# Kernel tuning notes

Measured on AMD Instinct MI355X. Metric: run time of the kernel, lower is better.

## Reference

```python
import jax, jax.numpy as jnp
import numpy as np

IN_FEATURES = 4096
OUT_FEATURES = 4096
TOKENS = 8192
QMAX = 127.0


def setup_inputs() -> dict:
    key = jax.random.key(0)
    k1, k2, k3, k4 = jax.random.split(key, 4)
    x = jax.random.normal(k1, (TOKENS, IN_FEATURES), dtype=jnp.float32)
    # int8 quantized weights in [-127, 127]
    Wq = jax.random.randint(k2, (OUT_FEATURES, IN_FEATURES), -127, 128, dtype=jnp.int32).astype(jnp.int8)
    # per-row absmax scales (positive)
    row_scales = jax.random.uniform(k3, (OUT_FEATURES,), dtype=jnp.float32, minval=0.01, maxval=1.0)
    bias_param = jax.random.normal(k4, (OUT_FEATURES,), dtype=jnp.float32)
    return {"x": x, "Wq": Wq, "row_scales": row_scales, "bias_param": bias_param}


def reference(x, Wq, row_scales, bias_param):
    # rowwise dequant: W[o, i] = Wq[o, i] * row_scales[o] / 127
    W_dequant = Wq.astype(x.dtype) * (row_scales.astype(x.dtype) / QMAX)[:, None]  # [O, I]
    Y = jnp.matmul(x, W_dequant.T)  # [T, O]
    return Y + bias_param.astype(x.dtype)
```

## Files before the change

### kernel.cpp

```cpp
#include <hip/hip_runtime.h>

#define M_TOK 8192
#define N_OUT 4096
#define K_IN  4096

#define AS1 __attribute__((address_space(1)))
#define AS3 __attribute__((address_space(3)))

typedef __attribute__((ext_vector_type(4))) int i32x4;
typedef __attribute__((ext_vector_type(16))) int i32x16;

template <int OFF>
__device__ __forceinline__ i32x4 dsri(unsigned addr) {
    i32x4 r;
    asm volatile("ds_read_b128 %0, %1 offset:%2" : "=v"(r) : "v"(addr), "n"(OFF));
    return r;
}


__global__ __launch_bounds__(256) void quant_x_kernel(
    const float* __restrict__ x, signed char* __restrict__ xq,
    float* __restrict__ tok_scale)
{
    const int row = blockIdx.x;
    const float4* xr = reinterpret_cast<const float4*>(x + (size_t)row * K_IN);
    const int t = threadIdx.x;
    float4 v[4];
    float m = 0.f;
#pragma unroll
    for (int i = 0; i < 4; ++i) {
        v[i] = xr[t + 256 * i];
        m = fmaxf(m, fmaxf(fmaxf(fabsf(v[i].x), fabsf(v[i].y)),
                           fmaxf(fabsf(v[i].z), fabsf(v[i].w))));
    }
#pragma unroll
    for (int off = 32; off >= 1; off >>= 1)
        m = fmaxf(m, __shfl_xor(m, off, 64));
    __shared__ float wmax[4];
    if ((t & 63) == 0) wmax[t >> 6] = m;
    __syncthreads();
    m = fmaxf(fmaxf(wmax[0], wmax[1]), fmaxf(wmax[2], wmax[3]));
    if (t == 0) tok_scale[row] = m * (1.0f / 127.0f);
    const float inv = (m > 0.f) ? (127.0f / m) : 0.f;
    int* xqi = reinterpret_cast<int*>(xq + (size_t)row * K_IN);
#pragma unroll
    for (int i = 0; i < 4; ++i) {
        const int q0 = __float2int_rn(v[i].x * inv) & 255;
        const int q1 = __float2int_rn(v[i].y * inv) & 255;
        const int q2 = __float2int_rn(v[i].z * inv) & 255;
        const int q3 = __float2int_rn(v[i].w * inv) & 255;
        xqi[t + 256 * i] = q0 | (q1 << 8) | (q2 << 16) | (q3 << 24);
    }
}


__global__ __launch_bounds__(256) void retile_x_kernel(
    const signed char* __restrict__ xq8, signed char* __restrict__ xqF)
{
    __shared__ __align__(16) char lds[32768];
    const int t = threadIdx.x;
    const int rb = blockIdx.x >> 2;
    const int kc = blockIdx.x & 3;

    const size_t srcBase = (size_t)rb * 32 * K_IN + (size_t)kc * 1024;
#pragma unroll
    for (int j = 0; j < 8; ++j) {
        const int u = j * 256 + t;
        const int row = u >> 6, gc = u & 63;
        const i32x4 v = *reinterpret_cast<const i32x4*>(
            xq8 + srcBase + (size_t)row * K_IN + gc * 16);
        *reinterpret_cast<i32x4*>(
            lds + ((row * 64 + (gc ^ (row & 7))) * 16)) = v;
    }
    __syncthreads();

    const int l = t & 63;
    const int W = t >> 6;
    const int row = l & 31;
    const int hi = l >> 5;
    i32x4* dst0 = reinterpret_cast<i32x4*>(xqF) +
                  ((size_t)rb * 128 + kc * 32) * 64 + l;
#pragma unroll
    for (int i = 0; i < 8; ++i) {
        const int kfl = W * 8 + i;
        const int gc = (kfl * 2 + hi) ^ (row & 7);
        const i32x4 v = *reinterpret_cast<const i32x4*>(
            lds + ((row * 64 + gc) * 16));
        dst0[(size_t)kfl * 64] = v;
    }
}


__global__ __launch_bounds__(256) void pack_w_frag_kernel(
    const int* __restrict__ wq, signed char* __restrict__ wqF)
{
    const int t = threadIdx.x;
    const int l = t & 63;
    const int W = t >> 6;
    const int rb = blockIdx.x >> 3;
    const int pc = blockIdx.x & 7;
    const int r = rb * 32 + (l & 31);
    const int4* wr4 = reinterpret_cast<const int4*>(wq) + (size_t)r * 1024;
    i32x4* outF = reinterpret_cast<i32x4*>(wqF) + (size_t)rb * 128 * 64 + l;
#pragma unroll
    for (int q = 0; q < 4; ++q) {
        const int f = W + 4 * (pc * 4 + q);
        const int c4 = f * 8 + (l >> 5) * 4;
        i32x4 o;
#pragma unroll
        for (int j = 0; j < 4; ++j) {
            const int4 a = wr4[c4 + j];
            o[j] = (a.x & 255) | ((a.y & 255) << 8) | ((a.z & 255) << 16) | ((a.w & 255) << 24);
        }
        outF[(size_t)f * 64] = o;
    }
}


#define NKT 128
#define SLOTA 8192
#define SLOTB 4096

#define MFMA(a, b, c) c = __builtin_amdgcn_mfma_i32_32x32x32_i8(a, b, c, 0, 0, 0)

#define RD6(P, aA, bA)                          \
    P##_B0 = dsri<0>(bA);                       \
    P##_B1 = dsri<1024>(bA);                    \
    P##_A0 = dsri<0>(aA);                       \
    P##_A1 = dsri<1024>(aA);                    \
    P##_A2 = dsri<2048>(aA);                    \
    P##_A3 = dsri<3072>(aA);

#define CL4a(P)                                               \
    MFMA(P##_A0, P##_B0, acc00); MFMA(P##_A0, P##_B1, acc01); \
    MFMA(P##_A1, P##_B0, acc10); MFMA(P##_A1, P##_B1, acc11);

#define CL4b(P)                                               \
    MFMA(P##_A2, P##_B0, acc20); MFMA(P##_A2, P##_B1, acc21); \
    MFMA(P##_A3, P##_B0, acc30); MFMA(P##_A3, P##_B1, acc31);

#define GBODY(T, C, N, DO_STAGE, VM)                                      \
    {                                                                     \
        asm volatile("s_waitcnt lgkmcnt(2)" ::: "memory");                \
        __builtin_amdgcn_sched_barrier(0);                                \
        __builtin_amdgcn_s_setprio(1);                                    \
        CL4a(C)                                                           \
        __builtin_amdgcn_s_setprio(0);                                    \
        __builtin_amdgcn_sched_barrier(0);                                \
        const unsigned aN_ = aBase + (unsigned)((((T) + 1) & 3) * SLOTA); \
        const unsigned bN_ = bBase + (unsigned)((((T) + 1) & 3) * SLOTB); \
        RD6(N, aN_, bN_)                                                  \
        if (DO_STAGE) stageAB((T) + 3);                                   \
        asm volatile("s_waitcnt lgkmcnt(6)" ::: "memory");                \
        __builtin_amdgcn_sched_barrier(0);                                \
        __builtin_amdgcn_s_setprio(1);                                    \
        CL4b(C)                                                           \
        __builtin_amdgcn_s_setprio(0);                                    \
        __builtin_amdgcn_sched_barrier(0);                                \
        asm volatile("s_waitcnt vmcnt(" #VM ")" ::: "memory");            \
        __builtin_amdgcn_sched_barrier(0);                                \
        __builtin_amdgcn_s_barrier();                                     \
        __builtin_amdgcn_sched_barrier(0);                                \
    }

#define GFINAL(C)                                                         \
    {                                                                     \
        asm volatile("s_waitcnt lgkmcnt(2)" ::: "memory");                \
        __builtin_amdgcn_sched_barrier(0);                                \
        __builtin_amdgcn_s_setprio(1);                                    \
        CL4a(C)                                                           \
        __builtin_amdgcn_s_setprio(0);                                    \
        asm volatile("s_waitcnt lgkmcnt(0)" ::: "memory");                \
        __builtin_amdgcn_sched_barrier(0);                                \
        __builtin_amdgcn_s_setprio(1);                                    \
        CL4b(C)                                                           \
        __builtin_amdgcn_s_setprio(0);                                    \
        __builtin_amdgcn_sched_barrier(0);                                \
    }

__global__ __launch_bounds__(256, 2) void qgemm_i8w4_kernel(
    const signed char* __restrict__ xqF,
    const signed char* __restrict__ wqF,
    const float* __restrict__ tok_scale,
    const float* __restrict__ row_scales,
    const float* __restrict__ bias,
    float* __restrict__ out)
{
    __shared__ __align__(16) char smem[49152];

    const int tid = threadIdx.x;
    const int l = tid & 63;
    const int w = tid >> 6;
    const int wr = w >> 1;
    const int wc = w & 1;

    const int bid = blockIdx.x;
    const int swz = (bid & 7) * 128 + (bid >> 3);
    const int bm = swz >> 5;
    const int bn = swz & 31;

    const signed char* aS0 = xqF + ((size_t)(bm * 8 + 2 * w) * 128) * 1024 + (size_t)l * 16;
    const signed char* bS  = wqF + ((size_t)(bn * 4 + w) * 128) * 1024 + (size_t)l * 16;
    char* aDst = smem + w * 2048;
    char* bDst = smem + 32768 + w * 1024;

    auto stageAB = [&](int tt) {
        const unsigned sa = (tt & 3) * SLOTA;
        const unsigned sb = (tt & 3) * SLOTB;
        __builtin_amdgcn_global_load_lds(
            (const AS1 void*)(aS0 + (size_t)tt * 1024),
            (AS3 void*)(aDst + sa), 16, 0, 0);
        __builtin_amdgcn_global_load_lds(
            (const AS1 void*)(aS0 + 131072 + (size_t)tt * 1024),
            (AS3 void*)(aDst + sa + 1024), 16, 0, 0);
        __builtin_amdgcn_global_load_lds(
            (const AS1 void*)(bS + (size_t)tt * 1024),
            (AS3 void*)(bDst + sb), 16, 0, 0);
    };

    const unsigned sbase = (unsigned)(uintptr_t)(AS3 char*)smem;
    const unsigned aBase = sbase + (unsigned)(wr * 4096 + l * 16);
    const unsigned bBase = sbase + 32768u + (unsigned)(wc * 2048 + l * 16);

    i32x16 acc00 = {0}, acc01 = {0}, acc10 = {0}, acc11 = {0};
    i32x16 acc20 = {0}, acc21 = {0}, acc30 = {0}, acc31 = {0};

    i32x4 X_A0, X_A1, X_A2, X_A3, X_B0, X_B1;
    i32x4 Y_A0, Y_A1, Y_A2, Y_A3, Y_B0, Y_B1;

    stageAB(0); stageAB(1); stageAB(2);
    asm volatile("s_waitcnt vmcnt(3)" ::: "memory");
    __builtin_amdgcn_sched_barrier(0);
    __builtin_amdgcn_s_barrier();
    __builtin_amdgcn_sched_barrier(0);
    RD6(X, aBase, bBase)

    for (int t = 0; t < 124; t += 2) {
        GBODY(t,     X, Y, true, 3);
        GBODY(t + 1, Y, X, true, 3);
    }
    GBODY(124, X, Y, true, 3);
    GBODY(125, Y, X, false, 0);
    GBODY(126, X, Y, false, 0);
    GFINAL(Y)

    const int cl = l & 31;
    const int rg4 = (l >> 5) * 4;
    const int gcol0 = bn * 128 + wc * 64;
    const float* tsrow = tok_scale + bm * 256 + wr * 128;
    float cs[2], bb[2];
#pragma unroll
    for (int nb = 0; nb < 2; ++nb) {
        const int col = gcol0 + nb * 32 + cl;
        cs[nb] = row_scales[col] * (1.0f / 127.0f);
        bb[nb] = bias[col];
    }
    const i32x16* accs[4][2] = {{&acc00, &acc01}, {&acc10, &acc11},
                                {&acc20, &acc21}, {&acc30, &acc31}};
#pragma unroll
    for (int mb = 0; mb < 4; ++mb) {
#pragma unroll
        for (int reg = 0; reg < 16; ++reg) {
            const int rl = mb * 32 + (reg & 3) + 8 * (reg >> 2) + rg4;
            const float tsv = tsrow[rl];
            float* orow = out + (size_t)(bm * 256 + wr * 128 + rl) * N_OUT + gcol0 + cl;
#pragma unroll
            for (int nb = 0; nb < 2; ++nb) {
                const int a = (*accs[mb][nb])[reg];
                orow[nb * 32] = (float)a * tsv * cs[nb] + bb[nb];
            }
        }
    }
}


extern "C" void kernel_launch(void* const* d_in, const int* in_sizes, int n_in,
                              void* d_out, int out_size, void* d_ws, size_t ws_size,
                              hipStream_t stream) {
    const float* x = (const float*)d_in[0];
    const int* wq = (const int*)d_in[1];
    const float* row_scales = (const float*)d_in[2];
    const float* bias = (const float*)d_in[3];
    float* out = (float*)d_out;

    signed char* xq8 = (signed char*)d_ws;
    signed char* xqF = xq8 + (size_t)M_TOK * K_IN;
    signed char* wqF = xqF + (size_t)M_TOK * K_IN;
    float* tok_scale = (float*)(wqF + (size_t)N_OUT * K_IN);
    (void)ws_size;

    quant_x_kernel<<<M_TOK, 256, 0, stream>>>(x, xq8, tok_scale);
    pack_w_frag_kernel<<<1024, 256, 0, stream>>>(wq, wqF);
    retile_x_kernel<<<1024, 256, 0, stream>>>(xq8, xqF);

    const int nblocks = (M_TOK / 256) * (N_OUT / 128);
    qgemm_i8w4_kernel<<<nblocks, 256, 0, stream>>>(
        xqF, wqF, tok_scale, row_scales, bias, out);
}
```

Measured before the change: 197.7 us.

## Shrink GEMM tile to 128x128 and raise occupancy to four blocks per CU

The int8 GEMM block tile drops from 256x128 to 128x128, halving the A staging buffers and per-wave accumulators so shared memory falls to 32KB and launch bounds allow four blocks per CU. The inner loop now issues one group of four MFMAs per k-step with a full LDS wait, instead of splitting eight MFMAs around the next fragment reads. The grid size, swizzle, and epilogue indexing are adjusted to match. This trades reuse of each loaded B tile and the intra-wave LDS/MFMA overlap for more resident waves to hide latency.

```diff
diff --git a/kernel.cpp b/kernel.cpp
--- a/kernel.cpp
+++ b/kernel.cpp
@@ -118,45 +118,33 @@
 
 
 #define NKT 128
-#define SLOTA 8192
+#define SLOTA 4096
 #define SLOTB 4096
 
 #define MFMA(a, b, c) c = __builtin_amdgcn_mfma_i32_32x32x32_i8(a, b, c, 0, 0, 0)
 
-#define RD6(P, aA, bA)                          \
-    P##_B0 = dsri<0>(bA);                       \
-    P##_B1 = dsri<1024>(bA);                    \
+#define RD4(P, aA, bA)                          \
     P##_A0 = dsri<0>(aA);                       \
     P##_A1 = dsri<1024>(aA);                    \
-    P##_A2 = dsri<2048>(aA);                    \
-    P##_A3 = dsri<3072>(aA);
-
-#define CL4a(P)                                               \
+    P##_B0 = dsri<0>(bA);                       \
+    P##_B1 = dsri<1024>(bA);
+
+#define CL4(P)                                                \
     MFMA(P##_A0, P##_B0, acc00); MFMA(P##_A0, P##_B1, acc01); \
     MFMA(P##_A1, P##_B0, acc10); MFMA(P##_A1, P##_B1, acc11);
 
-#define CL4b(P)                                               \
-    MFMA(P##_A2, P##_B0, acc20); MFMA(P##_A2, P##_B1, acc21); \
-    MFMA(P##_A3, P##_B0, acc30); MFMA(P##_A3, P##_B1, acc31);
-
 #define GBODY(T, C, N, DO_STAGE, VM)                                      \
     {                                                                     \
-        asm volatile("s_waitcnt lgkmcnt(2)" ::: "memory");                \
+        asm volatile("s_waitcnt lgkmcnt(0)" ::: "memory");                \
         __builtin_amdgcn_sched_barrier(0);                                \
         __builtin_amdgcn_s_setprio(1);                                    \
-        CL4a(C)                                                           \
+        CL4(C)                                                            \
         __builtin_amdgcn_s_setprio(0);                                    \
         __builtin_amdgcn_sched_barrier(0);                                \
         const unsigned aN_ = aBase + (unsigned)((((T) + 1) & 3) * SLOTA); \
         const unsigned bN_ = bBase + (unsigned)((((T) + 1) & 3) * SLOTB); \
-        RD6(N, aN_, bN_)                                                  \
+        RD4(N, aN_, bN_)                                                  \
         if (DO_STAGE) stageAB((T) + 3);                                   \
-        asm volatile("s_waitcnt lgkmcnt(6)" ::: "memory");                \
-        __builtin_amdgcn_sched_barrier(0);                                \
-        __builtin_amdgcn_s_setprio(1);                                    \
-        CL4b(C)                                                           \
-        __builtin_amdgcn_s_setprio(0);                                    \
-        __builtin_amdgcn_sched_barrier(0);                                \
         asm volatile("s_waitcnt vmcnt(" #VM ")" ::: "memory");            \
         __builtin_amdgcn_sched_barrier(0);                                \
         __builtin_amdgcn_s_barrier();                                     \
@@ -165,20 +153,15 @@
 
 #define GFINAL(C)                                                         \
     {                                                                     \
-        asm volatile("s_waitcnt lgkmcnt(2)" ::: "memory");                \
+        asm volatile("s_waitcnt lgkmcnt(0)" ::: "memory");                \
         __builtin_amdgcn_sched_barrier(0);                                \
         __builtin_amdgcn_s_setprio(1);                                    \
-        CL4a(C)                                                           \
+        CL4(C)                                                            \
         __builtin_amdgcn_s_setprio(0);                                    \
-        asm volatile("s_waitcnt lgkmcnt(0)" ::: "memory");                \
-        __builtin_amdgcn_sched_barrier(0);                                \
-        __builtin_amdgcn_s_setprio(1);                                    \
-        CL4b(C)                                                           \
-        __builtin_amdgcn_s_setprio(0);                                    \
-        __builtin_amdgcn_sched_barrier(0);                                \
-    }
-
-__global__ __launch_bounds__(256, 2) void qgemm_i8w4_kernel(
+        __builtin_amdgcn_sched_barrier(0);                                \
+    }
+
+__global__ __launch_bounds__(256, 4) void qgemm_i8o4_kernel(
     const signed char* __restrict__ xqF,
     const signed char* __restrict__ wqF,
     const float* __restrict__ tok_scale,
@@ -186,7 +169,7 @@
     const float* __restrict__ bias,
     float* __restrict__ out)
 {
-    __shared__ __align__(16) char smem[49152];
+    __shared__ __align__(16) char smem[32768];
 
     const int tid = threadIdx.x;
     const int l = tid & 63;
@@ -195,51 +178,45 @@
     const int wc = w & 1;
 
     const int bid = blockIdx.x;
-    const int swz = (bid & 7) * 128 + (bid >> 3);
+    const int swz = (bid & 7) * 256 + (bid >> 3);
     const int bm = swz >> 5;
     const int bn = swz & 31;
 
-    const signed char* aS0 = xqF + ((size_t)(bm * 8 + 2 * w) * 128) * 1024 + (size_t)l * 16;
-    const signed char* bS  = wqF + ((size_t)(bn * 4 + w) * 128) * 1024 + (size_t)l * 16;
-    char* aDst = smem + w * 2048;
-    char* bDst = smem + 32768 + w * 1024;
+    const signed char* aS = xqF + ((size_t)(bm * 4 + w) * 128) * 1024 + (size_t)l * 16;
+    const signed char* bS = wqF + ((size_t)(bn * 4 + w) * 128) * 1024 + (size_t)l * 16;
+    char* aDst = smem + w * 1024;
+    char* bDst = smem + 16384 + w * 1024;
 
     auto stageAB = [&](int tt) {
-        const unsigned sa = (tt & 3) * SLOTA;
-        const unsigned sb = (tt & 3) * SLOTB;
         __builtin_amdgcn_global_load_lds(
-            (const AS1 void*)(aS0 + (size_t)tt * 1024),
-            (AS3 void*)(aDst + sa), 16, 0, 0);
-        __builtin_amdgcn_global_load_lds(
-            (const AS1 void*)(aS0 + 131072 + (size_t)tt * 1024),
-            (AS3 void*)(aDst + sa + 1024), 16, 0, 0);
+            (const AS1 void*)(aS + (size_t)tt * 1024),
+            (AS3 void*)(aDst + (tt & 3) * SLOTA), 16, 0, 0);
         __builtin_amdgcn_global_load_lds(
             (const AS1 void*)(bS + (size_t)tt * 1024),
-            (AS3 void*)(bDst + sb), 16, 0, 0);
+            (AS3 void*)(bDst + (tt & 3) * SLOTB), 16, 0, 0);
     };
 
     const unsigned sbase = (unsigned)(uintptr_t)(AS3 char*)smem;
-    const unsigned aBase = sbase + (unsigned)(wr * 4096 + l * 16);
-    const unsigned bBase = sbase + 32768u + (unsigned)(wc * 2048 + l * 16);
+    const unsigned aBase = sbase + (unsigned)(wr * 2048 + l * 16);
+    const unsigned bBase = sbase + 16384u + (unsigned)(wc * 2048 + l * 16);
 
     i32x16 acc00 = {0}, acc01 = {0}, acc10 = {0}, acc11 = {0};
-    i32x16 acc20 = {0}, acc21 = {0}, acc30 = {0}, acc31 = {0};
-
-    i32x4 X_A0, X_A1, X_A2, X_A3, X_B0, X_B1;
-    i32x4 Y_A0, Y_A1, Y_A2, Y_A3, Y_B0, Y_B1;
+
+    i32x4 X_A0, X_A1, X_B0, X_B1;
+    i32x4 Y_A0, Y_A1, Y_B0, Y_B1;
 
     stageAB(0); stageAB(1); stageAB(2);
-    asm volatile("s_waitcnt vmcnt(3)" ::: "memory");
+    asm volatile("s_waitcnt vmcnt(2)" ::: "memory");
     __builtin_amdgcn_sched_barrier(0);
     __builtin_amdgcn_s_barrier();
     __builtin_amdgcn_sched_barrier(0);
-    RD6(X, aBase, bBase)
+    RD4(X, aBase, bBase)
 
     for (int t = 0; t < 124; t += 2) {
-        GBODY(t,     X, Y, true, 3);
-        GBODY(t + 1, Y, X, true, 3);
-    }
-    GBODY(124, X, Y, true, 3);
+        GBODY(t,     X, Y, true, 2);
+        GBODY(t + 1, Y, X, true, 2);
+    }
+    GBODY(124, X, Y, true, 2);
     GBODY(125, Y, X, false, 0);
     GBODY(126, X, Y, false, 0);
     GFINAL(Y)
@@ -247,7 +224,7 @@
     const int cl = l & 31;
     const int rg4 = (l >> 5) * 4;
     const int gcol0 = bn * 128 + wc * 64;
-    const float* tsrow = tok_scale + bm * 256 + wr * 128;
+    const float* tsrow = tok_scale + bm * 128 + wr * 64;
     float cs[2], bb[2];
 #pragma unroll
     for (int nb = 0; nb < 2; ++nb) {
@@ -255,15 +232,14 @@
         cs[nb] = row_scales[col] * (1.0f / 127.0f);
         bb[nb] = bias[col];
     }
-    const i32x16* accs[4][2] = {{&acc00, &acc01}, {&acc10, &acc11},
-                                {&acc20, &acc21}, {&acc30, &acc31}};
-#pragma unroll
-    for (int mb = 0; mb < 4; ++mb) {
+    const i32x16* accs[2][2] = {{&acc00, &acc01}, {&acc10, &acc11}};
+#pragma unroll
+    for (int mb = 0; mb < 2; ++mb) {
 #pragma unroll
         for (int reg = 0; reg < 16; ++reg) {
             const int rl = mb * 32 + (reg & 3) + 8 * (reg >> 2) + rg4;
             const float tsv = tsrow[rl];
-            float* orow = out + (size_t)(bm * 256 + wr * 128 + rl) * N_OUT + gcol0 + cl;
+            float* orow = out + (size_t)(bm * 128 + wr * 64 + rl) * N_OUT + gcol0 + cl;
 #pragma unroll
             for (int nb = 0; nb < 2; ++nb) {
                 const int a = (*accs[mb][nb])[reg];
@@ -293,7 +269,7 @@
     pack_w_frag_kernel<<<1024, 256, 0, stream>>>(wq, wqF);
     retile_x_kernel<<<1024, 256, 0, stream>>>(xq8, xqF);
 
-    const int nblocks = (M_TOK / 256) * (N_OUT / 128);
-    qgemm_i8w4_kernel<<<nblocks, 256, 0, stream>>>(
+    const int nblocks = (M_TOK / 128) * (N_OUT / 128);
+    qgemm_i8o4_kernel<<<nblocks, 256, 0, stream>>>(
         xqF, wqF, tok_scale, row_scales, bias, out);
 }
```

Result: slower. 223.4 us (+13.0%).
